# Kernel optimization log

Hardware: AMD Instinct MI355X
Metric: run time of the kernel (lower is better)

The kernel has to match this reference:

```python
import jax, jax.numpy as jnp
import numpy as np
from jax import lax

H, HD, P, C, HID = 8, 64, 16, 512, 2048
ALIBI_ALPHA, START_I = 1.0, 0
EPS = 1e-5

def setup_inputs():
    key = jax.random.key(0)
    ks = jax.random.split(key, 20)
    s = 0.02
    return {
        "x": jax.random.normal(ks[0], (8, 1024, C), jnp.float32),
        "Wq": jax.random.normal(ks[1], (HD, HD), jnp.float32) * s,
        "Wk": jax.random.normal(ks[2], (HD, HD), jnp.float32) * s,
        "Wv": jax.random.normal(ks[3], (HD, HD), jnp.float32) * s,
        "Wo": jax.random.normal(ks[4], (C, C), jnp.float32) * s,
        "bo": jnp.zeros((C,), jnp.float32),
        "th_pre": jax.random.normal(ks[5], (H, H), jnp.float32) * (1.0 / np.sqrt(H)),
        "th_post": jax.random.normal(ks[6], (H, H), jnp.float32) * (1.0 / np.sqrt(H)),
        "p_keys": jax.random.normal(ks[7], (P, 1, HD), jnp.float32) * s,
        "p_values": jax.random.normal(ks[8], (P, 1, HD), jnp.float32) * s,
        "conv1_w": jax.random.normal(ks[9], (2 * HID, C, 3), jnp.float32) * s,
        "conv1_b": jnp.zeros((2 * HID,), jnp.float32),
        "conv2_w": jax.random.normal(ks[10], (C, HID, 3), jnp.float32) * s,
        "conv2_b": jnp.zeros((C,), jnp.float32),
        "ln1_g": jnp.ones((C,), jnp.float32),
        "ln1_b": jnp.zeros((C,), jnp.float32),
        "ln2_g": jnp.ones((C,), jnp.float32),
        "ln2_b": jnp.zeros((C,), jnp.float32),
    }

def _layernorm(x, g, b):
    mu = jnp.mean(x, axis=-1, keepdims=True)
    var = jnp.mean((x - mu) ** 2, axis=-1, keepdims=True)
    return (x - mu) * lax.rsqrt(var + EPS) * g + b

def _mha(x, Wq, Wk, Wv, Wo, bo, th_pre, th_post, p_keys, p_values):
    N, L, _ = x.shape
    xh = x.reshape(N, L, H, HD)
    q = xh @ Wq.T  # per-head-dim linear, as in torch (applied to last dim)
    k = xh @ Wk.T
    v = xh @ Wv.T
    # persistent memory: [P,1,HD] broadcast over batch and heads
    pk = jnp.broadcast_to(p_keys[None], (N, P, H, HD))
    pv = jnp.broadcast_to(p_values[None], (N, P, H, HD))
    k = jnp.concatenate([k, pk], axis=1)  # (N, L+P, H, HD)
    v = jnp.concatenate([v, pv], axis=1)
    energy = jnp.einsum('nqhd,nkhd->nhqk', q, k)
    # ALiBi: slope_h = 2^(-alpha*(h+1+start_i)), bias = -|q-k|*slope, zero on persistent cols
    slopes = 2.0 ** (-ALIBI_ALPHA * (jnp.arange(1, H + 1, dtype=jnp.float32) + START_I))
    t = jnp.arange(L, dtype=jnp.float32)
    dist = jnp.abs(t[:, None] - t[None, :])  # (L, L)
    bias = -dist[None, :, :] * slopes[:, None, None]  # (H, L, L)
    bias = jnp.pad(bias, ((0, 0), (0, 0), (0, P)))
    energy = energy + bias[None]
    energy = jnp.einsum('gh,nhqk->ngqk', th_pre, energy)  # pre-softmax talking heads (1x1 conv)
    attn = jax.nn.softmax(energy / jnp.sqrt(jnp.float32(C)), axis=-1)
    attn = jnp.einsum('gh,nhqk->ngqk', th_post, attn)  # post-softmax talking heads
    out = jnp.einsum('nhql,nlhd->nqhd', attn, v).reshape(N, L, C)
    return out @ Wo.T + bo

def _ffn(x, conv1_w, conv1_b, conv2_w, conv2_b):
    dn = ('NCH', 'OIH', 'NCH')
    xc = jnp.transpose(x, (0, 2, 1))  # (N, C, L)
    xp = jnp.pad(xc, ((0, 0), (0, 0), (1, 1)))  # same padding, k=3
    h = lax.conv_general_dilated(xp, conv1_w, (1,), 'VALID', dimension_numbers=dn) + conv1_b[None, :, None]
    h1, h2 = jnp.split(h, 2, axis=1)
    h = jax.nn.silu(h1) * h2  # swiglu
    hp = jnp.pad(h, ((0, 0), (0, 0), (1, 1)))
    y = lax.conv_general_dilated(hp, conv2_w, (1,), 'VALID', dimension_numbers=dn) + conv2_b[None, :, None]
    return jnp.transpose(y, (0, 2, 1))

def reference(x, Wq, Wk, Wv, Wo, bo, th_pre, th_post, p_keys, p_values,
              conv1_w, conv1_b, conv2_w, conv2_b, ln1_g, ln1_b, ln2_g, ln2_b):
    a = _mha(x, Wq, Wk, Wv, Wo, bo, th_pre, th_post, p_keys, p_values)
    x1 = _layernorm(a + x, ln1_g, ln1_b)
    f = _ffn(x1, conv1_w, conv1_b, conv2_w, conv2_b)
    return _layernorm(f + x1, ln2_g, ln2_b)
```

## Files before the change

### kernel.cpp

```cpp
#include <hip/hip_runtime.h>
#include <cstddef>
#include <cstdint>

#define NB   8
#define LQ   1024
#define CH   512
#define HHE  8
#define HDD  64
#define PPM  16
#define LP   1040
#define HID  2048

typedef unsigned short ushort_t;
typedef __attribute__((ext_vector_type(8))) short short8;
typedef __attribute__((ext_vector_type(4))) float floatx4;

static const size_t O_QB   = 0;
static const size_t O_KB   = 2097152;
static const size_t O_VB   = 4227072;
static const size_t O_VT   = 6356992;
static const size_t O_AOB  = 8486912;
static const size_t O_AF   = 10584064;
static const size_t O_X1B  = 16777216;
static const size_t O_HPAD = 18878464;
static const size_t O_W1   = 27283456;
static const size_t O_W2   = 30429184;
static const size_t O_WO   = 32002048;

__device__ __forceinline__ ushort_t f2bf(float f) {
  uint32_t u = __float_as_uint(f);
  u += 0x7FFFu + ((u >> 16) & 1u);
  return (ushort_t)(u >> 16);
}
__device__ __forceinline__ float bf2f(ushort_t h) {
  return __uint_as_float(((uint32_t)h) << 16);
}

__device__ __forceinline__ void async16(ushort_t* lds, const ushort_t* g) {
  __builtin_amdgcn_global_load_lds(
      (const __attribute__((address_space(1))) void*)g,
      (__attribute__((address_space(3))) void*)lds, 16, 0, 0);
}

__global__ __launch_bounds__(256) void pack_bf16_kernel(
    const float* __restrict__ src, ushort_t* __restrict__ dst,
    int K, int KD, int icShift)
{
  const int oc = blockIdx.x;
  const int icMask = (1 << icShift) - 1;
  for (int k = threadIdx.x; k < K; k += 256) {
    int ic = k & icMask, dl = k >> icShift;
    dst[(size_t)oc * K + k] = f2bf(src[(size_t)oc * K + ic * KD + dl]);
  }
}

template<int EPI>
__global__ __launch_bounds__(256, 2) void mfma_gemm(
    const ushort_t* __restrict__ Ab, const ushort_t* __restrict__ Bb,
    int K, int BS, int P, int NOUT,
    const float* __restrict__ bias, const float* __restrict__ res,
    float* __restrict__ outf, ushort_t* __restrict__ outh)
{
  __shared__ ushort_t As[128 * 32];
  __shared__ ushort_t Bs[128 * 32];
  const int t = threadIdx.x;
  const int w = t >> 6, l = t & 63;
  const int m0 = blockIdx.x * 128, n0 = blockIdx.y * 128;

  const int sub = l >> 2;
  const int kc8 = (l & 3) * 8;
  const ushort_t* aptr[2];
  const ushort_t* bptr[2];
  #pragma unroll
  for (int c = 0; c < 2; ++c) {
    int arow = m0 + w * 32 + c * 16 + sub;
    aptr[c] = Ab + (size_t)(arow >> 10) * BS + (size_t)(arow & 1023) * P + kc8;
    int brow = n0 + w * 32 + c * 16 + sub;
    bptr[c] = Bb + (size_t)brow * K + kc8;
  }

  const int wm = w >> 1, wn = w & 1;
  const int lm = l & 15, q = l >> 4;
  floatx4 acc[4][4];
  #pragma unroll
  for (int i = 0; i < 4; ++i)
    #pragma unroll
    for (int j = 0; j < 4; ++j)
      acc[i][j] = (floatx4){0.f, 0.f, 0.f, 0.f};

  const int kIters = K >> 5;
  for (int kt = 0; kt < kIters; ++kt) {
    __syncthreads();
    async16(&As[w * 1024 +   0], aptr[0]);
    async16(&As[w * 1024 + 512], aptr[1]);
    async16(&Bs[w * 1024 +   0], bptr[0]);
    async16(&Bs[w * 1024 + 512], bptr[1]);
    aptr[0] += 32; aptr[1] += 32; bptr[0] += 32; bptr[1] += 32;
    __syncthreads();
    short8 af[4], bf[4];
    #pragma unroll
    for (int i = 0; i < 4; ++i)
      af[i] = *(const short8*)&As[(wm * 64 + i * 16 + lm) * 32 + q * 8];
    #pragma unroll
    for (int i = 0; i < 4; ++i)
      bf[i] = *(const short8*)&Bs[(wn * 64 + i * 16 + lm) * 32 + q * 8];
    #pragma unroll
    for (int i = 0; i < 4; ++i)
      #pragma unroll
      for (int j = 0; j < 4; ++j)
        acc[i][j] = __builtin_amdgcn_mfma_f32_16x16x32_bf16(af[i], bf[j], acc[i][j], 0, 0, 0);
  }

  #pragma unroll
  for (int i = 0; i < 4; ++i) {
    #pragma unroll
    for (int j = 0; j < 4; ++j) {
      const int mbase = m0 + wm * 64 + i * 16 + q * 4;
      const int n = n0 + wn * 64 + j * 16 + lm;
      #pragma unroll
      for (int r = 0; r < 4; ++r) {
        const int m = mbase + r;
        float v = acc[i][j][r];
        if (EPI == 0) {
          outh[(size_t)m * NOUT + n] = f2bf(v);
        } else if (EPI == 1) {
          outf[(size_t)m * NOUT + n] = v + bias[n];
        } else {
          outf[(size_t)m * NOUT + n] = v + bias[n] + res[(size_t)m * NOUT + n];
        }
      }
    }
  }
}

__global__ __launch_bounds__(256) void qkv_mfma(
    const float* __restrict__ x,
    const float* __restrict__ Wq, const float* __restrict__ Wk, const float* __restrict__ Wv,
    ushort_t* __restrict__ qo, ushort_t* __restrict__ ko, ushort_t* __restrict__ vo)
{
  __shared__ ushort_t Ws[8 * 512];
  const int mat = blockIdx.y;
  const float* __restrict__ W = (mat == 0) ? Wq : (mat == 1) ? Wk : Wv;
  const int t = threadIdx.x;

  for (int e = t; e < 4096; e += 256) {
    const int oc = e >> 6, ic = e & 63;
    const int nt = oc >> 4, lmm = oc & 15, s = ic >> 5, qd = (ic >> 3) & 3, j = ic & 7;
    Ws[(((nt * 2 + s) * 4 + qd) * 16 + lmm) * 8 + j] = f2bf(W[e]);
  }

  const int w = t >> 6, l = t & 63;
  const int lm = l & 15, quad = l >> 4;
  const int tok0 = blockIdx.x * 64 + w * 16;

  short8 af[16];
  {
    const float* xrow = x + (size_t)(tok0 + lm) * CH + quad * 8;
    #pragma unroll
    for (int h = 0; h < 8; ++h) {
      #pragma unroll
      for (int s = 0; s < 2; ++s) {
        const float4 a = *(const float4*)(xrow + h * 64 + s * 32);
        const float4 b = *(const float4*)(xrow + h * 64 + s * 32 + 4);
        short8 f;
        f[0] = (short)f2bf(a.x); f[1] = (short)f2bf(a.y);
        f[2] = (short)f2bf(a.z); f[3] = (short)f2bf(a.w);
        f[4] = (short)f2bf(b.x); f[5] = (short)f2bf(b.y);
        f[6] = (short)f2bf(b.z); f[7] = (short)f2bf(b.w);
        af[h * 2 + s] = f;
      }
    }
  }
  __syncthreads();

  short8 bfr[8];
  #pragma unroll
  for (int nt = 0; nt < 4; ++nt)
    #pragma unroll
    for (int s = 0; s < 2; ++s)
      bfr[nt * 2 + s] = *(const short8*)&Ws[((nt * 2 + s) * 64 + l) * 8];

  const int n = tok0 >> 10, lpos = tok0 & 1023;
  ushort_t* outp;
  size_t base;
  if (mat == 0) { base = ((size_t)n * LQ + lpos) * CH; outp = qo; }
  else          { base = ((size_t)n * LP + lpos) * CH; outp = (mat == 1) ? ko : vo; }

  #pragma unroll
  for (int h = 0; h < 8; ++h) {
    floatx4 acc[4];
    #pragma unroll
    for (int nt = 0; nt < 4; ++nt) acc[nt] = (floatx4){0.f, 0.f, 0.f, 0.f};
    #pragma unroll
    for (int nt = 0; nt < 4; ++nt)
      #pragma unroll
      for (int s = 0; s < 2; ++s)
        acc[nt] = __builtin_amdgcn_mfma_f32_16x16x32_bf16(
            af[h * 2 + s], bfr[nt * 2 + s], acc[nt], 0, 0, 0);
    #pragma unroll
    for (int nt = 0; nt < 4; ++nt)
      #pragma unroll
      for (int r = 0; r < 4; ++r)
        outp[base + (size_t)(quad * 4 + r) * CH + h * 64 + nt * 16 + lm] =
            f2bf(acc[nt][r]);
  }
}

__global__ __launch_bounds__(256) void persist_kernel(
    const float* __restrict__ pk, const float* __restrict__ pv,
    ushort_t* __restrict__ ko, ushort_t* __restrict__ vo)
{
  const int t = blockIdx.x * 256 + threadIdx.x;
  const int n = t >> 13, p = (t >> 9) & 15, c = t & 511, d = c & 63;
  const size_t o = ((size_t)n * LP + LQ + p) * CH + c;
  ko[o] = f2bf(pk[p * 64 + d]);
  vo[o] = f2bf(pv[p * 64 + d]);
}

__global__ __launch_bounds__(256) void vtrans_kernel(
    const ushort_t* __restrict__ Vb, ushort_t* __restrict__ VT)
{
  __shared__ ushort_t Ls[16 * 520];
  const int n = blockIdx.y, k0 = blockIdx.x * 16;
  const int t = threadIdx.x;
  const int r = t >> 4;
  {
    const ushort_t* src = Vb + ((size_t)(n * LP + k0 + r)) * 512 + (t & 15) * 8;
    ushort_t* dst = &Ls[r * 520 + (t & 15) * 8];
    #pragma unroll
    for (int it = 0; it < 4; ++it)
      *(short8*)(dst + it * 128) = *(const short8*)(src + it * 128);
  }
  __syncthreads();
  #pragma unroll
  for (int rep = 0; rep < 2; ++rep) {
    const int d = t + rep * 256;
    short8 v0, v1;
    #pragma unroll
    for (int j = 0; j < 8; ++j) {
      v0[j] = (short)Ls[j * 520 + d];
      v1[j] = (short)Ls[(8 + j) * 520 + d];
    }
    ushort_t* dst = VT + ((size_t)(n * 512 + d)) * LP + k0;
    *(short8*)(dst)     = v0;
    *(short8*)(dst + 8) = v1;
  }
}

__global__ __launch_bounds__(256, 2) void attn_mfma(
    const ushort_t* __restrict__ Qb, const ushort_t* __restrict__ Kb,
    const ushort_t* __restrict__ VT,
    const float* __restrict__ thpre, const float* __restrict__ thpost,
    ushort_t* __restrict__ aob)
{
  __shared__ ushort_t Ks[16 * 520];
  __shared__ ushort_t Vt[512 * 40];
  __shared__ float   Ps[8 * 16 * 36];
  const int n = blockIdx.y, q0 = blockIdx.x * 16;
  const int t = threadIdx.x;
  const int w = t >> 6, l = t & 63;
  const int lm = l & 15, quad = l >> 4;
  const float invs = 0.044194173824159216f;

  short8 qf[16];
  {
    const ushort_t* qrow = Qb + ((size_t)(n * LQ + q0 + lm)) * 512 + quad * 8;
    #pragma unroll
    for (int h = 0; h < 8; ++h) {
      qf[h * 2 + 0] = *(const short8*)(qrow + h * 64);
      qf[h * 2 + 1] = *(const short8*)(qrow + h * 64 + 32);
    }
  }
  float tps[2][8], psl[2], tpo[2][8];
  #pragma unroll
  for (int gg = 0; gg < 2; ++gg) {
    const int g = w * 2 + gg;
    float ps = 0.f;
    #pragma unroll
    for (int h = 0; h < 8; ++h) {
      float tv = thpre[g * 8 + h] * invs;
      tps[gg][h] = tv;
      ps += tv * (1.0f / (float)(2 << h));
      tpo[gg][h] = thpost[g * 8 + h];
    }
    psl[gg] = ps;
  }

  float m_[2][4], z_[2][4], zi[2][4];
  #pragma unroll
  for (int gg = 0; gg < 2; ++gg)
    #pragma unroll
    for (int r = 0; r < 4; ++r) { m_[gg][r] = -1e30f; z_[gg][r] = 0.f; }

  floatx4 o_[2][4];
  #pragma unroll
  for (int gg = 0; gg < 2; ++gg)
    #pragma unroll
    for (int ch = 0; ch < 4; ++ch) o_[gg][ch] = (floatx4){0.f, 0.f, 0.f, 0.f};

  const ushort_t* ksrc = Kb + ((size_t)(n * LP + (t >> 4))) * 512 + (t & 15) * 8;
  ushort_t* kdst = &Ks[(t >> 4) * 520 + (t & 15) * 8];
  const ushort_t* ksrc2;
  const ushort_t* vsA;
  const ushort_t* vsB;
  short8 kA[4], kB[4], vA[4], vB[4];
  const ushort_t* kbase = &Ks[lm * 520 + quad * 8];

  auto loadK = [&](short8 (&r)[4], const ushort_t* src) {
    #pragma unroll
    for (int it = 0; it < 4; ++it) r[it] = *(const short8*)(src + it * 128);
  };
  auto storeK = [&](short8 (&r)[4]) {
    #pragma unroll
    for (int it = 0; it < 4; ++it) *(short8*)(kdst + it * 128) = r[it];
  };
  auto loadV = [&](short8 (&r)[4]) {
    r[0] = *(const short8*)(vsA);  r[1] = *(const short8*)(vsA + 8);
    r[2] = *(const short8*)(vsB);  r[3] = *(const short8*)(vsB + 8);
    vsA += 16; vsB += 16;
  };
  auto storeV = [&](short8 (&r)[4], int sub) {
    ushort_t* d0 = &Vt[(size_t)t * 40 + sub * 16];
    ushort_t* d1 = &Vt[(size_t)(t + 256) * 40 + sub * 16];
    *(short8*)(d0)     = r[0]; *(short8*)(d0 + 8) = r[1];
    *(short8*)(d1)     = r[2]; *(short8*)(d1 + 8) = r[3];
  };

  auto qkt = [&](floatx4 (&ef)[8]) {
    #pragma unroll
    for (int h = 0; h < 8; ++h) {
      floatx4 e = (floatx4){0.f, 0.f, 0.f, 0.f};
      short8 b0 = *(const short8*)(kbase + h * 64);
      short8 b1 = *(const short8*)(kbase + h * 64 + 32);
      e = __builtin_amdgcn_mfma_f32_16x16x32_bf16(qf[h * 2 + 0], b0, e, 0, 0, 0);
      e = __builtin_amdgcn_mfma_f32_16x16x32_bf16(qf[h * 2 + 1], b1, e, 0, 0, 0);
      ef[h] = e;
    }
  };

  auto p1_compute = [&](int step) {
    floatx4 ef[8];
    qkt(ef);
    const int k0 = step * 16;
    const bool alibi = (step < 64);
    #pragma unroll
    for (int r = 0; r < 4; ++r) {
      const float dist = fabsf((float)(q0 + quad * 4 + r - (k0 + lm)));
      #pragma unroll
      for (int gg = 0; gg < 2; ++gg) {
        float s = tps[gg][0] * ef[0][r];
        #pragma unroll
        for (int h = 1; h < 8; ++h) s += tps[gg][h] * ef[h][r];
        if (alibi) s -= dist * psl[gg];
        const float mo = m_[gg][r];
        const float mn = fmaxf(mo, s);
        z_[gg][r] = z_[gg][r] * __expf(mo - mn) + __expf(s - mn);
        m_[gg][r] = mn;
      }
    }
  };

  auto p2_compute = [&](int step, int sub) {
    floatx4 ef[8];
    qkt(ef);
    const int k0 = step * 16;
    const bool alibi = (step < 64);
    #pragma unroll
    for (int r = 0; r < 4; ++r) {
      const float dist = fabsf((float)(q0 + quad * 4 + r - (k0 + lm)));
      #pragma unroll
      for (int gg = 0; gg < 2; ++gg) {
        float s = tps[gg][0] * ef[0][r];
        #pragma unroll
        for (int h = 1; h < 8; ++h) s += tps[gg][h] * ef[h][r];
        if (alibi) s -= dist * psl[gg];
        const float p = __expf(s - m_[gg][r]) * zi[gg][r];
        Ps[((w * 2 + gg) * 16 + quad * 4 + r) * 36 + sub * 16 + lm] = p;
        if (step == 64)
          Ps[((w * 2 + gg) * 16 + quad * 4 + r) * 36 + 16 + lm] = 0.f;
      }
    }
  };

  auto mix_av = [&]() {
    float pm[2][8];
    #pragma unroll
    for (int gg = 0; gg < 2; ++gg)
      #pragma unroll
      for (int j = 0; j < 8; ++j) pm[gg][j] = 0.f;
    #pragma unroll
    for (int g = 0; g < 8; ++g) {
      const float4 pa = *(const float4*)&Ps[(g * 16 + lm) * 36 + quad * 8];
      const float4 pb = *(const float4*)&Ps[(g * 16 + lm) * 36 + quad * 8 + 4];
      #pragma unroll
      for (int gg = 0; gg < 2; ++gg) {
        const float tw = tpo[gg][g];
        pm[gg][0] += tw * pa.x; pm[gg][1] += tw * pa.y;
        pm[gg][2] += tw * pa.z; pm[gg][3] += tw * pa.w;
        pm[gg][4] += tw * pb.x; pm[gg][5] += tw * pb.y;
        pm[gg][6] += tw * pb.z; pm[gg][7] += tw * pb.w;
      }
    }
    short8 pk[2];
    #pragma unroll
    for (int gg = 0; gg < 2; ++gg)
      #pragma unroll
      for (int j = 0; j < 8; ++j) pk[gg][j] = (short)f2bf(pm[gg][j]);
    #pragma unroll
    for (int gg = 0; gg < 2; ++gg) {
      #pragma unroll
      for (int ch = 0; ch < 4; ++ch) {
        const int d = (w * 2 + gg) * 64 + ch * 16 + lm;
        const short8 vf = *(const short8*)&Vt[d * 40 + quad * 8];
        o_[gg][ch] = __builtin_amdgcn_mfma_f32_16x16x32_bf16(pk[gg], vf, o_[gg][ch], 0, 0, 0);
      }
    }
  };

  auto p2_step = [&](short8 (&kc)[4], short8 (&vc)[4],
                     short8 (&kn)[4], short8 (&vn)[4], int step, int sub) {
    __syncthreads();
    storeK(kc);
    storeV(vc, sub);
    if (step < 64) {
      loadK(kn, ksrc2); ksrc2 += 8192;
      loadV(vn);
    }
    __syncthreads();
    p2_compute(step, sub);
  };

  loadK(kA, ksrc); ksrc += 8192;
  for (int s = 0; s < 64; s += 2) {
    __syncthreads();
    storeK(kA);
    loadK(kB, ksrc); ksrc += 8192;
    __syncthreads();
    p1_compute(s);

    __syncthreads();
    storeK(kB);
    loadK(kA, ksrc); ksrc += 8192;
    __syncthreads();
    p1_compute(s + 1);
  }
  ksrc2 = Kb + ((size_t)(n * LP + (t >> 4))) * 512 + (t & 15) * 8;
  vsA   = VT + ((size_t)(n * 512 + t)) * LP;
  vsB   = VT + ((size_t)(n * 512 + t + 256)) * LP;
  __syncthreads();
  storeK(kA);
  loadK(kB, ksrc2); ksrc2 += 8192;
  loadV(vA);
  __syncthreads();
  p1_compute(64);

  #pragma unroll
  for (int off = 1; off < 16; off <<= 1) {
    #pragma unroll
    for (int gg = 0; gg < 2; ++gg)
      #pragma unroll
      for (int r = 0; r < 4; ++r) {
        const float mo = __shfl_xor(m_[gg][r], off);
        const float zo = __shfl_xor(z_[gg][r], off);
        const float mn = fmaxf(m_[gg][r], mo);
        z_[gg][r] = z_[gg][r] * __expf(m_[gg][r] - mn) + zo * __expf(mo - mn);
        m_[gg][r] = mn;
      }
  }
  #pragma unroll
  for (int gg = 0; gg < 2; ++gg)
    #pragma unroll
    for (int r = 0; r < 4; ++r) zi[gg][r] = 1.0f / z_[gg][r];

  for (int pair = 0; pair < 32; ++pair) {
    p2_step(kB, vA, kA, vB, 2 * pair,     0);
    p2_step(kA, vB, kB, vA, 2 * pair + 1, 1);
    __syncthreads();
    mix_av();
  }
  p2_step(kB, vA, kA, vB, 64, 0);
  __syncthreads();
  mix_av();

  #pragma unroll
  for (int gg = 0; gg < 2; ++gg)
    #pragma unroll
    for (int ch = 0; ch < 4; ++ch) {
      const int d = (w * 2 + gg) * 64 + ch * 16 + lm;
      #pragma unroll
      for (int r = 0; r < 4; ++r)
        aob[((size_t)(n * LQ + q0 + quad * 4 + r)) * 512 + d] = f2bf(o_[gg][ch][r]);
    }
}

__global__ __launch_bounds__(256) void swiglu_kernel(
    const ushort_t* __restrict__ hraw, const float* __restrict__ bias,
    ushort_t* __restrict__ hpad)
{
  const int tok = blockIdx.x;
  const int n = tok >> 10, l = tok & 1023;
  const size_t src = (size_t)tok * 4096;
  const size_t dst = ((size_t)n * 1026 + l + 1) * 2048;
  for (int c = threadIdx.x; c < 2048; c += 256) {
    float h1 = bf2f(hraw[src + c]) + bias[c];
    float h2 = bf2f(hraw[src + 2048 + c]) + bias[2048 + c];
    float s = h1 / (1.f + __expf(-h1));
    hpad[dst + c] = f2bf(s * h2);
  }
}

__global__ __launch_bounds__(256) void zero_pads_kernel(
    ushort_t* __restrict__ x1b, ushort_t* __restrict__ hpad)
{
  const int b = blockIdx.x;
  const int n = b >> 1, side = b & 1;
  const size_t r = (size_t)n * 1026 + side * 1025;
  ushort2 z; z.x = 0; z.y = 0;
  *(ushort2*)&x1b[r * 512 + threadIdx.x * 2] = z;
  #pragma unroll
  for (int i = 0; i < 4; ++i)
    *(ushort2*)&hpad[r * 2048 + (threadIdx.x + 256 * i) * 2] = z;
}

__global__ __launch_bounds__(256) void ln_kernel(
    const float* __restrict__ in, const float* __restrict__ res,
    const float* __restrict__ g, const float* __restrict__ b,
    float* __restrict__ outp, ushort_t* __restrict__ bfout)
{
  const int w = threadIdx.x >> 6, lane = threadIdx.x & 63;
  const int tok = blockIdx.x * 4 + w;
  const size_t base = (size_t)tok * CH;
  float4 v0 = *(const float4*)&in[base + (lane << 2)];
  float4 v1 = *(const float4*)&in[base + 256 + (lane << 2)];
  if (res != nullptr) {
    float4 r0 = *(const float4*)&res[base + (lane << 2)];
    float4 r1 = *(const float4*)&res[base + 256 + (lane << 2)];
    v0.x += r0.x; v0.y += r0.y; v0.z += r0.z; v0.w += r0.w;
    v1.x += r1.x; v1.y += r1.y; v1.z += r1.z; v1.w += r1.w;
  }
  float s = v0.x + v0.y + v0.z + v0.w + v1.x + v1.y + v1.z + v1.w;
  #pragma unroll
  for (int off = 32; off > 0; off >>= 1) s += __shfl_xor(s, off);
  const float mu = s * (1.f / 512.f);
  float d0 = v0.x - mu, d1 = v0.y - mu, d2 = v0.z - mu, d3 = v0.w - mu;
  float d4 = v1.x - mu, d5 = v1.y - mu, d6 = v1.z - mu, d7 = v1.w - mu;
  float vs = d0*d0 + d1*d1 + d2*d2 + d3*d3 + d4*d4 + d5*d5 + d6*d6 + d7*d7;
  #pragma unroll
  for (int off = 32; off > 0; off >>= 1) vs += __shfl_xor(vs, off);
  const float r = rsqrtf(vs * (1.f / 512.f) + 1e-5f);
  float4 ga = *(const float4*)&g[(lane << 2)];
  float4 gb = *(const float4*)&g[256 + (lane << 2)];
  float4 ba = *(const float4*)&b[(lane << 2)];
  float4 bb = *(const float4*)&b[256 + (lane << 2)];
  float4 o0, o1;
  o0.x = d0 * r * ga.x + ba.x; o0.y = d1 * r * ga.y + ba.y;
  o0.z = d2 * r * ga.z + ba.z; o0.w = d3 * r * ga.w + ba.w;
  o1.x = d4 * r * gb.x + bb.x; o1.y = d5 * r * gb.y + bb.y;
  o1.z = d6 * r * gb.z + bb.z; o1.w = d7 * r * gb.w + bb.w;
  *(float4*)&outp[base + (lane << 2)] = o0;
  *(float4*)&outp[base + 256 + (lane << 2)] = o1;
  if (bfout != nullptr) {
    const int n = tok >> 10, ll = tok & 1023;
    const size_t bb2 = ((size_t)n * 1026 + ll + 1) * 512;
    ushort4 u0 = make_ushort4(f2bf(o0.x), f2bf(o0.y), f2bf(o0.z), f2bf(o0.w));
    ushort4 u1 = make_ushort4(f2bf(o1.x), f2bf(o1.y), f2bf(o1.z), f2bf(o1.w));
    *(ushort4*)&bfout[bb2 + (lane << 2)] = u0;
    *(ushort4*)&bfout[bb2 + 256 + (lane << 2)] = u1;
  }
}

extern "C" void kernel_launch(void* const* d_in, const int* in_sizes, int n_in,
                              void* d_out, int out_size, void* d_ws, size_t ws_size,
                              hipStream_t stream)
{
  (void)in_sizes; (void)n_in; (void)out_size; (void)ws_size;
  const float* x      = (const float*)d_in[0];
  const float* Wq     = (const float*)d_in[1];
  const float* Wk     = (const float*)d_in[2];
  const float* Wv     = (const float*)d_in[3];
  const float* Wo     = (const float*)d_in[4];
  const float* bo     = (const float*)d_in[5];
  const float* th_pre = (const float*)d_in[6];
  const float* th_post= (const float*)d_in[7];
  const float* p_keys = (const float*)d_in[8];
  const float* p_vals = (const float*)d_in[9];
  const float* c1w    = (const float*)d_in[10];
  const float* c1b    = (const float*)d_in[11];
  const float* c2w    = (const float*)d_in[12];
  const float* c2b    = (const float*)d_in[13];
  const float* ln1g   = (const float*)d_in[14];
  const float* ln1b   = (const float*)d_in[15];
  const float* ln2g   = (const float*)d_in[16];
  const float* ln2b   = (const float*)d_in[17];

  float* ws  = (float*)d_ws;
  float* out = (float*)d_out;

  ushort_t* Qb   = (ushort_t*)(ws + O_QB);
  ushort_t* Kb   = (ushort_t*)(ws + O_KB);
  ushort_t* Vb   = (ushort_t*)(ws + O_VB);
  ushort_t* VT   = (ushort_t*)(ws + O_VT);
  ushort_t* aob  = (ushort_t*)(ws + O_AOB);
  float*    abf  = ws + O_AF;
  float*    fbf  = abf;
  ushort_t* x1b  = (ushort_t*)(ws + O_X1B);
  ushort_t* hpad = (ushort_t*)(ws + O_HPAD);
  ushort_t* hraw = (ushort_t*)ws;
  ushort_t* w1p  = (ushort_t*)(ws + O_W1);
  ushort_t* w2p  = (ushort_t*)(ws + O_W2);
  ushort_t* wop  = (ushort_t*)(ws + O_WO);

  pack_bf16_kernel<<<4096, 256, 0, stream>>>(c1w, w1p, 1536, 3, 9);
  pack_bf16_kernel<<<512,  256, 0, stream>>>(c2w, w2p, 6144, 3, 11);
  pack_bf16_kernel<<<512,  256, 0, stream>>>(Wo,  wop, 512,  1, 9);

  qkv_mfma<<<dim3(128, 3), 256, 0, stream>>>(x, Wq, Wk, Wv, Qb, Kb, Vb);
  persist_kernel<<<256, 256, 0, stream>>>(p_keys, p_vals, Kb, Vb);
  vtrans_kernel<<<dim3(65, 8), 256, 0, stream>>>(Vb, VT);

  attn_mfma<<<dim3(64, 8), 256, 0, stream>>>(Qb, Kb, VT, th_pre, th_post, aob);

  mfma_gemm<2><<<dim3(64, 4), 256, 0, stream>>>(
      aob, wop, 512, 1024 * 512, 512, 512, bo, x, abf, nullptr);

  ln_kernel<<<2048, 256, 0, stream>>>(abf, nullptr, ln1g, ln1b, out, x1b);
  zero_pads_kernel<<<16, 256, 0, stream>>>(x1b, hpad);

  mfma_gemm<0><<<dim3(64, 32), 256, 0, stream>>>(
      x1b, w1p, 1536, 1026 * 512, 512, 4096, nullptr, nullptr, nullptr, hraw);

  swiglu_kernel<<<8192, 256, 0, stream>>>(hraw, c1b, hpad);

  mfma_gemm<1><<<dim3(64, 4), 256, 0, stream>>>(
      hpad, w2p, 6144, 1026 * 2048, 2048, 512, c2b, nullptr, fbf, nullptr);

  ln_kernel<<<2048, 256, 0, stream>>>(fbf, out, ln2g, ln2b, out, nullptr);
}
```

Baseline: 656.8 us.

## Split QK^T heads across waves, exchange per-head energies via shared memory

Each wave now computes QK^T only for its own two heads, loading its K fragments straight from global memory into registers, so K is no longer staged through shared memory. The per-head energy tiles go to a double-buffered shared Eb array and are read back by all waves for the talking-heads mix. This removes the 4x redundant QK^T MFMA work and the K shared-memory round trip, and halves the barriers per step by handling two key steps per sync. In exchange it adds shared-memory traffic for the energy tiles, extra LDS footprint, and uncoalesced per-lane K loads from global memory.

Result: faster. 636.1 us (-3.2%).

```diff
diff --git a/kernel.cpp b/kernel.cpp
--- a/kernel.cpp
+++ b/kernel.cpp
@@ -253,24 +253,24 @@
     const float* __restrict__ thpre, const float* __restrict__ thpost,
     ushort_t* __restrict__ aob)
 {
-  __shared__ ushort_t Ks[16 * 520];
   __shared__ ushort_t Vt[512 * 40];
-  __shared__ float   Ps[8 * 16 * 36];
+  __shared__ float    Ps[8 * 16 * 36];
+  __shared__ __align__(16) float Eb[2][8 * 16 * 20];
   const int n = blockIdx.y, q0 = blockIdx.x * 16;
   const int t = threadIdx.x;
   const int w = t >> 6, l = t & 63;
   const int lm = l & 15, quad = l >> 4;
   const float invs = 0.044194173824159216f;
 
-  short8 qf[16];
+  short8 qf[4];
   {
-    const ushort_t* qrow = Qb + ((size_t)(n * LQ + q0 + lm)) * 512 + quad * 8;
-    #pragma unroll
-    for (int h = 0; h < 8; ++h) {
-      qf[h * 2 + 0] = *(const short8*)(qrow + h * 64);
-      qf[h * 2 + 1] = *(const short8*)(qrow + h * 64 + 32);
-    }
-  }
+    const ushort_t* qrow = Qb + ((size_t)(n * LQ + q0 + lm)) * 512 + (w * 2) * 64 + quad * 8;
+    qf[0] = *(const short8*)(qrow);
+    qf[1] = *(const short8*)(qrow + 32);
+    qf[2] = *(const short8*)(qrow + 64);
+    qf[3] = *(const short8*)(qrow + 96);
+  }
+
   float tps[2][8], psl[2], tpo[2][8];
   #pragma unroll
   for (int gg = 0; gg < 2; ++gg) {
@@ -298,26 +298,22 @@
     #pragma unroll
     for (int ch = 0; ch < 4; ++ch) o_[gg][ch] = (floatx4){0.f, 0.f, 0.f, 0.f};
 
-  const ushort_t* ksrc = Kb + ((size_t)(n * LP + (t >> 4))) * 512 + (t & 15) * 8;
-  ushort_t* kdst = &Ks[(t >> 4) * 520 + (t & 15) * 8];
-  const ushort_t* ksrc2;
-  const ushort_t* vsA;
-  const ushort_t* vsB;
-  short8 kA[4], kB[4], vA[4], vB[4];
-  const ushort_t* kbase = &Ks[lm * 520 + quad * 8];
-
-  auto loadK = [&](short8 (&r)[4], const ushort_t* src) {
-    #pragma unroll
-    for (int it = 0; it < 4; ++it) r[it] = *(const short8*)(src + it * 128);
+  const ushort_t* kg  = Kb + ((size_t)(n * LP + lm)) * 512 + (w * 2) * 64 + quad * 8;
+  const ushort_t* vgA = VT + ((size_t)(n * 512) + t) * LP;
+  const ushort_t* vgB = VT + ((size_t)(n * 512) + t + 256) * LP;
+
+  short8 kfE[4], kfO[4], vX[4], vY[4];
+
+  auto loadKg = [&](short8 (&r)[4], int step) {
+    const ushort_t* p = kg + (size_t)step * 8192;
+    r[0] = *(const short8*)(p);
+    r[1] = *(const short8*)(p + 32);
+    r[2] = *(const short8*)(p + 64);
+    r[3] = *(const short8*)(p + 96);
   };
-  auto storeK = [&](short8 (&r)[4]) {
-    #pragma unroll
-    for (int it = 0; it < 4; ++it) *(short8*)(kdst + it * 128) = r[it];
-  };
-  auto loadV = [&](short8 (&r)[4]) {
-    r[0] = *(const short8*)(vsA);  r[1] = *(const short8*)(vsA + 8);
-    r[2] = *(const short8*)(vsB);  r[3] = *(const short8*)(vsB + 8);
-    vsA += 16; vsB += 16;
+  auto loadVg = [&](short8 (&r)[4], int off) {
+    r[0] = *(const short8*)(vgA + off); r[1] = *(const short8*)(vgA + off + 8);
+    r[2] = *(const short8*)(vgB + off); r[3] = *(const short8*)(vgB + off + 8);
   };
   auto storeV = [&](short8 (&r)[4], int sub) {
     ushort_t* d0 = &Vt[(size_t)t * 40 + sub * 16];
@@ -326,21 +322,21 @@
     *(short8*)(d1)     = r[2]; *(short8*)(d1 + 8) = r[3];
   };
 
-  auto qkt = [&](floatx4 (&ef)[8]) {
-    #pragma unroll
-    for (int h = 0; h < 8; ++h) {
+  auto qktE = [&](short8 (&kf)[4], int buf) {
+    #pragma unroll
+    for (int hh = 0; hh < 2; ++hh) {
       floatx4 e = (floatx4){0.f, 0.f, 0.f, 0.f};
-      short8 b0 = *(const short8*)(kbase + h * 64);
-      short8 b1 = *(const short8*)(kbase + h * 64 + 32);
-      e = __builtin_amdgcn_mfma_f32_16x16x32_bf16(qf[h * 2 + 0], b0, e, 0, 0, 0);
-      e = __builtin_amdgcn_mfma_f32_16x16x32_bf16(qf[h * 2 + 1], b1, e, 0, 0, 0);
-      ef[h] = e;
+      e = __builtin_amdgcn_mfma_f32_16x16x32_bf16(qf[hh * 2 + 0], kf[hh * 2 + 0], e, 0, 0, 0);
+      e = __builtin_amdgcn_mfma_f32_16x16x32_bf16(qf[hh * 2 + 1], kf[hh * 2 + 1], e, 0, 0, 0);
+      *(floatx4*)&Eb[buf][(((w * 2 + hh) * 16 + lm)) * 20 + quad * 4] = e;
     }
   };
 
-  auto p1_compute = [&](int step) {
-    floatx4 ef[8];
-    qkt(ef);
+  auto mixP1 = [&](int step, int buf) {
+    floatx4 e4[8];
+    #pragma unroll
+    for (int h = 0; h < 8; ++h)
+      e4[h] = *(const floatx4*)&Eb[buf][(h * 16 + lm) * 20 + quad * 4];
     const int k0 = step * 16;
     const bool alibi = (step < 64);
     #pragma unroll
@@ -348,9 +344,9 @@
       const float dist = fabsf((float)(q0 + quad * 4 + r - (k0 + lm)));
       #pragma unroll
       for (int gg = 0; gg < 2; ++gg) {
-        float s = tps[gg][0] * ef[0][r];
+        float s = tps[gg][0] * e4[0][r];
         #pragma unroll
-        for (int h = 1; h < 8; ++h) s += tps[gg][h] * ef[h][r];
+        for (int h = 1; h < 8; ++h) s += tps[gg][h] * e4[h][r];
         if (alibi) s -= dist * psl[gg];
         const float mo = m_[gg][r];
         const float mn = fmaxf(mo, s);
@@ -360,9 +356,11 @@
     }
   };
 
-  auto p2_compute = [&](int step, int sub) {
-    floatx4 ef[8];
-    qkt(ef);
+  auto pCompute = [&](int step, int sub, int buf) {
+    floatx4 e4[8];
+    #pragma unroll
+    for (int h = 0; h < 8; ++h)
+      e4[h] = *(const floatx4*)&Eb[buf][(h * 16 + lm) * 20 + quad * 4];
     const int k0 = step * 16;
     const bool alibi = (step < 64);
     #pragma unroll
@@ -370,9 +368,9 @@
       const float dist = fabsf((float)(q0 + quad * 4 + r - (k0 + lm)));
       #pragma unroll
       for (int gg = 0; gg < 2; ++gg) {
-        float s = tps[gg][0] * ef[0][r];
+        float s = tps[gg][0] * e4[0][r];
         #pragma unroll
-        for (int h = 1; h < 8; ++h) s += tps[gg][h] * ef[h][r];
+        for (int h = 1; h < 8; ++h) s += tps[gg][h] * e4[h][r];
         if (alibi) s -= dist * psl[gg];
         const float p = __expf(s - m_[gg][r]) * zi[gg][r];
         Ps[((w * 2 + gg) * 16 + quad * 4 + r) * 36 + sub * 16 + lm] = p;
@@ -417,42 +415,26 @@
     }
   };
 
-  auto p2_step = [&](short8 (&kc)[4], short8 (&vc)[4],
-                     short8 (&kn)[4], short8 (&vn)[4], int step, int sub) {
+  loadKg(kfE, 0);
+  loadKg(kfO, 1);
+  for (int s = 0; s < 64; s += 2) {
+    qktE(kfE, 0);
+    qktE(kfO, 1);
+    loadKg(kfE, s + 2);
+    if (s + 3 <= 64) loadKg(kfO, s + 3);
     __syncthreads();
-    storeK(kc);
-    storeV(vc, sub);
-    if (step < 64) {
-      loadK(kn, ksrc2); ksrc2 += 8192;
-      loadV(vn);
-    }
+    mixP1(s, 0);
+    mixP1(s + 1, 1);
     __syncthreads();
-    p2_compute(step, sub);
-  };
-
-  loadK(kA, ksrc); ksrc += 8192;
-  for (int s = 0; s < 64; s += 2) {
-    __syncthreads();
-    storeK(kA);
-    loadK(kB, ksrc); ksrc += 8192;
-    __syncthreads();
-    p1_compute(s);
-
-    __syncthreads();
-    storeK(kB);
-    loadK(kA, ksrc); ksrc += 8192;
-    __syncthreads();
-    p1_compute(s + 1);
-  }
-  ksrc2 = Kb + ((size_t)(n * LP + (t >> 4))) * 512 + (t & 15) * 8;
-  vsA   = VT + ((size_t)(n * 512 + t)) * LP;
-  vsB   = VT + ((size_t)(n * 512 + t + 256)) * LP;
+  }
+  qktE(kfE, 0);
   __syncthreads();
-  storeK(kA);
-  loadK(kB, ksrc2); ksrc2 += 8192;
-  loadV(vA);
-  __syncthreads();
-  p1_compute(64);
+  mixP1(64, 0);
+
+  loadKg(kfE, 0);
+  loadKg(kfO, 1);
+  loadVg(vX, 0);
+  loadVg(vY, 16);
 
   #pragma unroll
   for (int off = 1; off < 16; off <<= 1) {
@@ -472,13 +454,27 @@
     #pragma unroll
     for (int r = 0; r < 4; ++r) zi[gg][r] = 1.0f / z_[gg][r];
 
-  for (int pair = 0; pair < 32; ++pair) {
-    p2_step(kB, vA, kA, vB, 2 * pair,     0);
-    p2_step(kA, vB, kB, vA, 2 * pair + 1, 1);
+  __syncthreads();
+
+  for (int p = 0; p < 32; ++p) {
+    qktE(kfE, 0);
+    qktE(kfO, 1);
+    loadKg(kfE, 2 * p + 2);
+    if (p < 31) loadKg(kfO, 2 * p + 3);
+    __syncthreads();
+    pCompute(2 * p,     0, 0);
+    pCompute(2 * p + 1, 1, 1);
+    storeV(vX, 0);
+    storeV(vY, 1);
+    loadVg(vX, 32 * (p + 1));
+    if (p < 31) loadVg(vY, 32 * (p + 1) + 16);
     __syncthreads();
     mix_av();
   }
-  p2_step(kB, vA, kA, vB, 64, 0);
+  qktE(kfE, 0);
+  __syncthreads();
+  pCompute(64, 0, 0);
+  storeV(vX, 0);
   __syncthreads();
   mix_av();
 
```
